# Kernel tuning notes

Measured on AMD Instinct MI355X. Metric: run time of the kernel, lower is better.

Reference implementation:

```python
import jax, jax.numpy as jnp
import numpy as np

IN_FEATURES = 4096
OUT_FEATURES = 4096
LORA_R = 64
LORA_ALPHA = 16
SCALING = LORA_ALPHA / LORA_R  # 0.25


def setup_inputs() -> dict:
    key = jax.random.key(0)
    k_x, k_w, k_s, k_a, k_b = jax.random.split(key, 5)
    x = jax.random.normal(k_x, (4, 2048, IN_FEATURES), dtype=jnp.float32)
    # int8 quantized base weight in [-8, 7] as in the torch buffer init
    weight_quantized = jax.random.randint(k_w, (OUT_FEATURES, IN_FEATURES), -8, 7, dtype=jnp.int8)
    weight_scale = jax.random.normal(k_s, (1,), dtype=jnp.float32)
    lora_A = jax.random.normal(k_a, (LORA_R, IN_FEATURES), dtype=jnp.float32) * 0.01
    # torch init is zeros; use small random values so the LoRA path is exercised
    lora_B = jax.random.normal(k_b, (OUT_FEATURES, LORA_R), dtype=jnp.float32) * 0.01
    return {"x": x, "weight_quantized": weight_quantized, "weight_scale": weight_scale,
            "lora_A": lora_A, "lora_B": lora_B}


def reference(x, weight_quantized, weight_scale, lora_A, lora_B):
    # 1. dequantize base weight on the fly: [out, in]
    w_dequant = weight_quantized.astype(x.dtype) * weight_scale
    # 2. base GEMM: [B, S, in] x [in, out] -> [B, S, out]
    base = jnp.einsum('bsi,oi->bso', x, w_dequant)
    # 3. LoRA low-rank update (dropout is identity in eval mode)
    lora = jnp.einsum('bsr,or->bso', jnp.einsum('bsi,ri->bsr', x, lora_A), lora_B)
    return base + lora * SCALING
```

## Files before the change

kernel.cpp:

```cpp
#include <hip/hip_runtime.h>

#define M_TOT 8192
#define K_TOT 4096
#define N_TOT 4096
#define RANK  64
#define SCALING 0.25f

typedef __bf16 bf16x8 __attribute__((ext_vector_type(8)));
typedef float floatx4 __attribute__((ext_vector_type(4)));
typedef float floatx16 __attribute__((ext_vector_type(16)));
typedef unsigned short ushort8v __attribute__((ext_vector_type(8)));

static __device__ __forceinline__ unsigned short f32_to_bf16(float f) {
  unsigned int u = __float_as_uint(f);
  u += 0x7FFFu + ((u >> 16) & 1u);
  return (unsigned short)(u >> 16);
}

static __device__ __forceinline__ void async_ld16(const void* g, void* l) {
  __builtin_amdgcn_global_load_lds(
      (const __attribute__((address_space(1))) unsigned int*)g,
      (__attribute__((address_space(3))) unsigned int*)l, 16, 0, 0);
}

__global__ __launch_bounds__(256) void cvt_x_kernel(const float4* __restrict__ x,
                                                    ushort8v* __restrict__ xb) {
  int i = blockIdx.x * 256 + threadIdx.x;
  float4 v0 = x[2 * i];
  float4 v1 = x[2 * i + 1];
  ushort8v o;
  o[0] = f32_to_bf16(v0.x); o[1] = f32_to_bf16(v0.y);
  o[2] = f32_to_bf16(v0.z); o[3] = f32_to_bf16(v0.w);
  o[4] = f32_to_bf16(v1.x); o[5] = f32_to_bf16(v1.y);
  o[6] = f32_to_bf16(v1.z); o[7] = f32_to_bf16(v1.w);
  xb[i] = o;
}

__global__ __launch_bounds__(256) void build_weff_kernel(
    const int* __restrict__ wq, const float* __restrict__ scale_p,
    const float* __restrict__ A, const float* __restrict__ B,
    unsigned short* __restrict__ Weff) {
  __shared__ __align__(16) float Bts[64][128];
  __shared__ __align__(16) float As_[64][128];

  const int tid = threadIdx.x;
  const int bo = blockIdx.y * 128;
  const int bk = blockIdx.x * 128;
  const float scale = scale_p[0];

  {
    const int o = tid >> 1;
    const int rh = (tid & 1) * 32;
    const float* gb = B + (size_t)(bo + o) * RANK + rh;
#pragma unroll
    for (int j = 0; j < 8; ++j) {
      float4 v = *(const float4*)(gb + j * 4);
      Bts[rh + j * 4 + 0][o] = v.x;
      Bts[rh + j * 4 + 1][o] = v.y;
      Bts[rh + j * 4 + 2][o] = v.z;
      Bts[rh + j * 4 + 3][o] = v.w;
    }
  }
#pragma unroll
  for (int j = 0; j < 8; ++j) {
    const int ii = j * 1024 + tid * 4;
    const int r = ii >> 7, c = ii & 127;
    *(floatx4*)&As_[r][c] = *(const floatx4*)(A + (size_t)r * K_TOT + bk + c);
  }
  __syncthreads();

  const int to = tid >> 4;
  const int tk = tid & 15;
  float acc[8][8] = {};
#pragma unroll 4
  for (int r = 0; r < RANK; ++r) {
    floatx4 b0 = *(const floatx4*)&Bts[r][to * 8];
    floatx4 b1 = *(const floatx4*)&Bts[r][to * 8 + 4];
    floatx4 a0 = *(const floatx4*)&As_[r][tk * 8];
    floatx4 a1 = *(const floatx4*)&As_[r][tk * 8 + 4];
    float bv[8] = {b0.x, b0.y, b0.z, b0.w, b1.x, b1.y, b1.z, b1.w};
    float av[8] = {a0.x, a0.y, a0.z, a0.w, a1.x, a1.y, a1.z, a1.w};
#pragma unroll
    for (int a = 0; a < 8; ++a)
#pragma unroll
      for (int b = 0; b < 8; ++b) acc[a][b] += bv[a] * av[b];
  }

#pragma unroll
  for (int a = 0; a < 8; ++a) {
    const int o = bo + to * 8 + a;
    const size_t base = (size_t)o * K_TOT + bk + tk * 8;
    const int4 w0 = *(const int4*)(wq + base);
    const int4 w1 = *(const int4*)(wq + base + 4);
    ushort8v st;
    st[0] = f32_to_bf16((float)w0.x * scale + SCALING * acc[a][0]);
    st[1] = f32_to_bf16((float)w0.y * scale + SCALING * acc[a][1]);
    st[2] = f32_to_bf16((float)w0.z * scale + SCALING * acc[a][2]);
    st[3] = f32_to_bf16((float)w0.w * scale + SCALING * acc[a][3]);
    st[4] = f32_to_bf16((float)w1.x * scale + SCALING * acc[a][4]);
    st[5] = f32_to_bf16((float)w1.y * scale + SCALING * acc[a][5]);
    st[6] = f32_to_bf16((float)w1.z * scale + SCALING * acc[a][6]);
    st[7] = f32_to_bf16((float)w1.w * scale + SCALING * acc[a][7]);
    *(ushort8v*)(Weff + base) = st;
  }
}

__global__ __launch_bounds__(512, 2) void gemm_kernel(
    const unsigned short* __restrict__ Xb,
    const unsigned short* __restrict__ Wb,
    float* __restrict__ out) {
  __shared__ __align__(16) unsigned char smem[131072];

  const int tid = threadIdx.x;
  const int lane = tid & 63;
  const int wave = tid >> 6;
  const int wm = wave >> 2;
  const int wn = wave & 3;

  const int bid = blockIdx.x;
  const int swz = (bid & 7) * 64 + (bid >> 3);
  const int bM = (swz >> 4) * 256;
  const int bN = (swz & 15) * 256;

  const int srow = tid >> 3;
  const int scol = ((tid & 7) ^ (srow & 7)) * 8;
  const unsigned short* xs = Xb + (size_t)(bM + srow) * K_TOT + scol;
  const unsigned short* ws = Wb + (size_t)(bN + srow) * K_TOT + scol;

  const int hi = lane >> 5;
  const int l7 = lane & 7;
  const int rb = (lane & 31) * 128;
  const int cc0 = ((0 * 2 + hi) ^ l7) * 16;
  const int cc1 = ((1 * 2 + hi) ^ l7) * 16;
  const int cc2 = ((2 * 2 + hi) ^ l7) * 16;
  const int cc3 = ((3 * 2 + hi) ^ l7) * 16;
  const int aBase = wm * 16384;
  const int bBase = 32768 + wn * 8192;

  floatx16 acc[4][2] = {};
  bf16x8 af[2][2];
  bf16x8 bf[2][4];

#define BAR() asm volatile("s_barrier" ::: "memory")
#define WAIT_LGKM0() asm volatile("s_waitcnt lgkmcnt(0)" ::: "memory")
#define WAIT_VM(N) asm volatile("s_waitcnt vmcnt(" #N ")" ::: "memory")
#define STAGE_A(BUF, H, S, KO)                                              \
  async_ld16(xs + (size_t)((H) * 128 + (S) * 64) * K_TOT + (KO),            \
             smem + (BUF) * 65536 + (H) * 16384 + (S) * 8192 + tid * 16)
#define STAGE_B(BUF, H, S, KO)                                              \
  async_ld16(ws + (size_t)((H) * 128 + (S) * 64) * K_TOT + (KO),            \
             smem + (BUF) * 65536 + 32768 + (H) * 16384 + (S) * 8192 + tid * 16)
#define RD_A(BUF, MI, MM, KK, CC)                                           \
  af[MM][KK] = *(const bf16x8*)(smem + (BUF) * 65536 + aBase + (MI) * 4096 + rb + (CC))
#define RD_B(BUF, NJ, KS, CC)                                               \
  bf[NJ][KS] = *(const bf16x8*)(smem + (BUF) * 65536 + bBase + (NJ) * 4096 + rb + (CC))

#define MFMA_OCT(MB, PB)                                                    \
  {                                                                         \
    _Pragma("unroll") for (int kk = 0; kk < 2; ++kk)                        \
    _Pragma("unroll") for (int mm = 0; mm < 2; ++mm)                        \
    _Pragma("unroll") for (int nn = 0; nn < 2; ++nn)                        \
      acc[(MB) + mm][nn] = __builtin_amdgcn_mfma_f32_32x32x16_bf16(         \
          af[mm][kk], bf[nn][kk + (PB)], acc[(MB) + mm][nn], 0, 0, 0);      \
  }

#define GROUP(BUF, KA, KB)                                                  \
  {                                                                         \
                            \
    RD_B(BUF, 0, 0, cc0); RD_B(BUF, 1, 0, cc0);                             \
    RD_A(BUF, 0, 0, 0, cc0); RD_A(BUF, 1, 1, 0, cc0);                       \
    RD_B(BUF, 0, 1, cc1); RD_B(BUF, 1, 1, cc1);                             \
    RD_A(BUF, 0, 0, 1, cc1); RD_A(BUF, 1, 1, 1, cc1);                       \
    STAGE_A((BUF) ^ 1, 0, 0, KA); STAGE_A((BUF) ^ 1, 0, 1, KA);             \
    __builtin_amdgcn_s_setprio(1);                                          \
    MFMA_OCT(0, 0);                                                         \
    __builtin_amdgcn_s_setprio(0);                                          \
    WAIT_LGKM0(); BAR();                                                    \
                            \
    RD_B(BUF, 0, 2, cc2); RD_B(BUF, 1, 2, cc2);                             \
    RD_A(BUF, 0, 0, 0, cc2); RD_A(BUF, 1, 1, 0, cc2);                       \
    RD_B(BUF, 0, 3, cc3); RD_B(BUF, 1, 3, cc3);                             \
    RD_A(BUF, 0, 0, 1, cc3); RD_A(BUF, 1, 1, 1, cc3);                       \
    STAGE_A((BUF) ^ 1, 1, 0, KA); STAGE_A((BUF) ^ 1, 1, 1, KA);             \
    __builtin_amdgcn_s_setprio(1);                                          \
    MFMA_OCT(0, 2);                                                         \
    __builtin_amdgcn_s_setprio(0);                                          \
    WAIT_LGKM0(); BAR();                                                    \
     \
    RD_A(BUF, 2, 0, 0, cc0); RD_A(BUF, 3, 1, 0, cc0);                       \
    RD_A(BUF, 2, 0, 1, cc1); RD_A(BUF, 3, 1, 1, cc1);                       \
    STAGE_B(BUF, 0, 0, KB); STAGE_B(BUF, 0, 1, KB);                         \
    __builtin_amdgcn_s_setprio(1);                                          \
    MFMA_OCT(2, 0);                                                         \
    __builtin_amdgcn_s_setprio(0);                                          \
    WAIT_LGKM0(); BAR();                                                    \
                 \
    RD_A(BUF, 2, 0, 0, cc2); RD_A(BUF, 3, 1, 0, cc2);                       \
    RD_A(BUF, 2, 0, 1, cc3); RD_A(BUF, 3, 1, 1, cc3);                       \
    STAGE_B(BUF, 1, 0, KB); STAGE_B(BUF, 1, 1, KB);                         \
    __builtin_amdgcn_s_setprio(1);                                          \
    MFMA_OCT(2, 2);                                                         \
    __builtin_amdgcn_s_setprio(0);                                          \
    WAIT_VM(4);                                                             \
    BAR();                                                                  \
  }

  STAGE_A(0, 0, 0, 0); STAGE_A(0, 0, 1, 0);
  STAGE_A(0, 1, 0, 0); STAGE_A(0, 1, 1, 0);
  STAGE_B(0, 0, 0, 0); STAGE_B(0, 0, 1, 0);
  STAGE_B(0, 1, 0, 0); STAGE_B(0, 1, 1, 0);
  STAGE_B(1, 0, 0, 64); STAGE_B(1, 0, 1, 64);
  STAGE_B(1, 1, 0, 64); STAGE_B(1, 1, 1, 64);
  WAIT_VM(0);
  BAR();

  for (int kt = 0; kt < 64; kt += 2) {
    const int ka0 = ((kt + 1) & 63) * 64;
    const int kb0 = ((kt + 2) & 63) * 64;
    const int ka1 = ((kt + 2) & 63) * 64;
    const int kb1 = ((kt + 3) & 63) * 64;
    GROUP(0, ka0, kb0);
    GROUP(1, ka1, kb1);
  }
  WAIT_VM(0);

  const int col0 = bN + wn * 64 + (lane & 31);
#pragma unroll
  for (int mi = 0; mi < 4; ++mi) {
    const int rbase = bM + wm * 128 + mi * 32 + hi * 4;
#pragma unroll
    for (int nj = 0; nj < 2; ++nj) {
#pragma unroll
      for (int rg = 0; rg < 4; ++rg)
#pragma unroll
        for (int rr = 0; rr < 4; ++rr)
          out[(size_t)(rbase + rg * 8 + rr) * N_TOT + (col0 + nj * 32)] =
              acc[mi][nj][rg * 4 + rr];
    }
  }
#undef BAR
#undef WAIT_LGKM0
#undef WAIT_VM
#undef STAGE_A
#undef STAGE_B
#undef RD_A
#undef RD_B
#undef MFMA_OCT
#undef GROUP
}

extern "C" void kernel_launch(void* const* d_in, const int* in_sizes, int n_in,
                              void* d_out, int out_size, void* d_ws, size_t ws_size,
                              hipStream_t stream) {
  const float* x      = (const float*)d_in[0];
  const int*   wq     = (const int*)d_in[1];
  const float* wscale = (const float*)d_in[2];
  const float* lora_A = (const float*)d_in[3];
  const float* lora_B = (const float*)d_in[4];
  float* out = (float*)d_out;

  unsigned short* xb   = (unsigned short*)d_ws;
  unsigned short* weff = (unsigned short*)((char*)d_ws + (size_t)M_TOT * K_TOT * 2);

  cvt_x_kernel<<<16384, 256, 0, stream>>>((const float4*)x, (ushort8v*)xb);
  build_weff_kernel<<<dim3(K_TOT / 128, N_TOT / 128), 256, 0, stream>>>(
      wq, wscale, lora_A, lora_B, weff);
  gemm_kernel<<<512, 512, 0, stream>>>(xb, weff, out);
}
```

Before: 525.9 us.

## Switch GEMM inner loop to 16x16x32 MFMA with two-phase schedule

Replaces the 32x32x16 bf16 MFMA tiling with 16x16x32 MFMAs, giving each wave an 8x4 grid of 16x16 accumulators, and changes the LDS fragment addressing and swizzle offsets to match. The four barrier-separated sub-phases per k-tile become two phases (ALPHA, BETA), each issuing all of its A or B global-to-LDS stages at the start, followed by a larger batch of LDS reads and MFMAs. The aim is fewer barriers and better MFMA issue density per synchronisation. In exchange it performs more LDS reads per MFMA and needs more fragment registers, which could hurt occupancy or increase LDS bandwidth pressure.

```diff
diff --git a/kernel.cpp b/kernel.cpp
--- a/kernel.cpp
+++ b/kernel.cpp
@@ -8,7 +8,6 @@
 
 typedef __bf16 bf16x8 __attribute__((ext_vector_type(8)));
 typedef float floatx4 __attribute__((ext_vector_type(4)));
-typedef float floatx16 __attribute__((ext_vector_type(16)));
 typedef unsigned short ushort8v __attribute__((ext_vector_type(8)));
 
 static __device__ __forceinline__ unsigned short f32_to_bf16(float f) {
@@ -105,6 +104,21 @@
   }
 }
 
+
+template <int QM>
+static __device__ __forceinline__ void mfma_half(floatx4 (&acc)[8][4],
+                                                 const bf16x8 (&af)[4][2],
+                                                 const bf16x8 (&bf)[4][2]) {
+#pragma unroll
+  for (int ks = 0; ks < 2; ++ks)
+#pragma unroll
+    for (int i = 0; i < 4; ++i)
+#pragma unroll
+      for (int j = 0; j < 4; ++j)
+        acc[QM * 4 + i][j] = __builtin_amdgcn_mfma_f32_16x16x32_bf16(
+            af[i][ks], bf[j][ks], acc[QM * 4 + i][j], 0, 0, 0);
+}
+
 __global__ __launch_bounds__(512, 2) void gemm_kernel(
     const unsigned short* __restrict__ Xb,
     const unsigned short* __restrict__ Wb,
@@ -127,19 +141,15 @@
   const unsigned short* xs = Xb + (size_t)(bM + srow) * K_TOT + scol;
   const unsigned short* ws = Wb + (size_t)(bN + srow) * K_TOT + scol;
 
-  const int hi = lane >> 5;
-  const int l7 = lane & 7;
-  const int rb = (lane & 31) * 128;
-  const int cc0 = ((0 * 2 + hi) ^ l7) * 16;
-  const int cc1 = ((1 * 2 + hi) ^ l7) * 16;
-  const int cc2 = ((2 * 2 + hi) ^ l7) * 16;
-  const int cc3 = ((3 * 2 + hi) ^ l7) * 16;
+  const int rb = (lane & 15) * 128;
+  const int c0 = (((lane >> 4) + 0) ^ (lane & 7)) * 16;
+  const int c1 = (((lane >> 4) + 4) ^ (lane & 7)) * 16;
   const int aBase = wm * 16384;
   const int bBase = 32768 + wn * 8192;
 
-  floatx16 acc[4][2] = {};
-  bf16x8 af[2][2];
-  bf16x8 bf[2][4];
+  floatx4 acc[8][4] = {};
+  bf16x8 af[4][2];
+  bf16x8 bf[4][2];
 
 #define BAR() asm volatile("s_barrier" ::: "memory")
 #define WAIT_LGKM0() asm volatile("s_waitcnt lgkmcnt(0)" ::: "memory")
@@ -150,59 +160,43 @@
 #define STAGE_B(BUF, H, S, KO)                                              \
   async_ld16(ws + (size_t)((H) * 128 + (S) * 64) * K_TOT + (KO),            \
              smem + (BUF) * 65536 + 32768 + (H) * 16384 + (S) * 8192 + tid * 16)
-#define RD_A(BUF, MI, MM, KK, CC)                                           \
-  af[MM][KK] = *(const bf16x8*)(smem + (BUF) * 65536 + aBase + (MI) * 4096 + rb + (CC))
-#define RD_B(BUF, NJ, KS, CC)                                               \
-  bf[NJ][KS] = *(const bf16x8*)(smem + (BUF) * 65536 + bBase + (NJ) * 4096 + rb + (CC))
-
-#define MFMA_OCT(MB, PB)                                                    \
+#define DSR_A(BUF, QM, II, KS)                                              \
+  af[II][KS] = *(const bf16x8*)(smem + (BUF) * 65536 + aBase +              \
+                                ((QM) * 4 + (II)) * 2048 + rb + ((KS) ? c1 : c0))
+#define DSR_B(BUF, J, KS)                                                   \
+  bf[J][KS] = *(const bf16x8*)(smem + (BUF) * 65536 + bBase +               \
+                               (J) * 2048 + rb + ((KS) ? c1 : c0))
+
+#define ALPHA(BUF, KA)                                                      \
   {                                                                         \
-    _Pragma("unroll") for (int kk = 0; kk < 2; ++kk)                        \
-    _Pragma("unroll") for (int mm = 0; mm < 2; ++mm)                        \
-    _Pragma("unroll") for (int nn = 0; nn < 2; ++nn)                        \
-      acc[(MB) + mm][nn] = __builtin_amdgcn_mfma_f32_32x32x16_bf16(         \
-          af[mm][kk], bf[nn][kk + (PB)], acc[(MB) + mm][nn], 0, 0, 0);      \
-  }
-
-#define GROUP(BUF, KA, KB)                                                  \
-  {                                                                         \
-                            \
-    RD_B(BUF, 0, 0, cc0); RD_B(BUF, 1, 0, cc0);                             \
-    RD_A(BUF, 0, 0, 0, cc0); RD_A(BUF, 1, 1, 0, cc0);                       \
-    RD_B(BUF, 0, 1, cc1); RD_B(BUF, 1, 1, cc1);                             \
-    RD_A(BUF, 0, 0, 1, cc1); RD_A(BUF, 1, 1, 1, cc1);                       \
     STAGE_A((BUF) ^ 1, 0, 0, KA); STAGE_A((BUF) ^ 1, 0, 1, KA);             \
+    STAGE_A((BUF) ^ 1, 1, 0, KA); STAGE_A((BUF) ^ 1, 1, 1, KA);             \
+    DSR_B(BUF, 0, 0); DSR_B(BUF, 1, 0);                                     \
+    DSR_A(BUF, 0, 0, 0); DSR_A(BUF, 0, 1, 0);                               \
+    DSR_B(BUF, 2, 0); DSR_B(BUF, 3, 0);                                     \
+    DSR_A(BUF, 0, 2, 0); DSR_A(BUF, 0, 3, 0);                               \
+    DSR_B(BUF, 0, 1); DSR_B(BUF, 1, 1);                                     \
+    DSR_A(BUF, 0, 0, 1); DSR_A(BUF, 0, 1, 1);                               \
+    DSR_B(BUF, 2, 1); DSR_B(BUF, 3, 1);                                     \
+    DSR_A(BUF, 0, 2, 1); DSR_A(BUF, 0, 3, 1);                               \
     __builtin_amdgcn_s_setprio(1);                                          \
-    MFMA_OCT(0, 0);                                                         \
+    mfma_half<0>(acc, af, bf);                                              \
     __builtin_amdgcn_s_setprio(0);                                          \
     WAIT_LGKM0(); BAR();                                                    \
-                            \
-    RD_B(BUF, 0, 2, cc2); RD_B(BUF, 1, 2, cc2);                             \
-    RD_A(BUF, 0, 0, 0, cc2); RD_A(BUF, 1, 1, 0, cc2);                       \
-    RD_B(BUF, 0, 3, cc3); RD_B(BUF, 1, 3, cc3);                             \
-    RD_A(BUF, 0, 0, 1, cc3); RD_A(BUF, 1, 1, 1, cc3);                       \
-    STAGE_A((BUF) ^ 1, 1, 0, KA); STAGE_A((BUF) ^ 1, 1, 1, KA);             \
+  }
+
+#define BETA(BUF, KB)                                                       \
+  {                                                                         \
+    STAGE_B(BUF, 0, 0, KB); STAGE_B(BUF, 0, 1, KB);                         \
+    STAGE_B(BUF, 1, 0, KB); STAGE_B(BUF, 1, 1, KB);                         \
+    DSR_A(BUF, 1, 0, 0); DSR_A(BUF, 1, 1, 0);                               \
+    DSR_A(BUF, 1, 2, 0); DSR_A(BUF, 1, 3, 0);                               \
+    DSR_A(BUF, 1, 0, 1); DSR_A(BUF, 1, 1, 1);                               \
+    DSR_A(BUF, 1, 2, 1); DSR_A(BUF, 1, 3, 1);                               \
     __builtin_amdgcn_s_setprio(1);                                          \
-    MFMA_OCT(0, 2);                                                         \
+    mfma_half<1>(acc, af, bf);                                              \
     __builtin_amdgcn_s_setprio(0);                                          \
-    WAIT_LGKM0(); BAR();                                                    \
-     \
-    RD_A(BUF, 2, 0, 0, cc0); RD_A(BUF, 3, 1, 0, cc0);                       \
-    RD_A(BUF, 2, 0, 1, cc1); RD_A(BUF, 3, 1, 1, cc1);                       \
-    STAGE_B(BUF, 0, 0, KB); STAGE_B(BUF, 0, 1, KB);                         \
-    __builtin_amdgcn_s_setprio(1);                                          \
-    MFMA_OCT(2, 0);                                                         \
-    __builtin_amdgcn_s_setprio(0);                                          \
-    WAIT_LGKM0(); BAR();                                                    \
-                 \
-    RD_A(BUF, 2, 0, 0, cc2); RD_A(BUF, 3, 1, 0, cc2);                       \
-    RD_A(BUF, 2, 0, 1, cc3); RD_A(BUF, 3, 1, 1, cc3);                       \
-    STAGE_B(BUF, 1, 0, KB); STAGE_B(BUF, 1, 1, KB);                         \
-    __builtin_amdgcn_s_setprio(1);                                          \
-    MFMA_OCT(2, 2);                                                         \
-    __builtin_amdgcn_s_setprio(0);                                          \
-    WAIT_VM(4);                                                             \
-    BAR();                                                                  \
+    WAIT_LGKM0(); WAIT_VM(4); BAR();                                        \
   }
 
   STAGE_A(0, 0, 0, 0); STAGE_A(0, 0, 1, 0);
@@ -219,23 +213,21 @@
     const int kb0 = ((kt + 2) & 63) * 64;
     const int ka1 = ((kt + 2) & 63) * 64;
     const int kb1 = ((kt + 3) & 63) * 64;
-    GROUP(0, ka0, kb0);
-    GROUP(1, ka1, kb1);
+    ALPHA(0, ka0); BETA(0, kb0);
+    ALPHA(1, ka1); BETA(1, kb1);
   }
   WAIT_VM(0);
 
-  const int col0 = bN + wn * 64 + (lane & 31);
-#pragma unroll
-  for (int mi = 0; mi < 4; ++mi) {
-    const int rbase = bM + wm * 128 + mi * 32 + hi * 4;
-#pragma unroll
-    for (int nj = 0; nj < 2; ++nj) {
-#pragma unroll
-      for (int rg = 0; rg < 4; ++rg)
-#pragma unroll
-        for (int rr = 0; rr < 4; ++rr)
-          out[(size_t)(rbase + rg * 8 + rr) * N_TOT + (col0 + nj * 32)] =
-              acc[mi][nj][rg * 4 + rr];
+  const int row0 = bM + wm * 128 + ((lane >> 4) << 2);
+  const int col0 = bN + wn * 64 + (lane & 15);
+#pragma unroll
+  for (int i = 0; i < 8; ++i) {
+#pragma unroll
+    for (int j = 0; j < 4; ++j) {
+#pragma unroll
+      for (int r = 0; r < 4; ++r) {
+        out[(size_t)(row0 + i * 16 + r) * N_TOT + (col0 + j * 16)] = acc[i][j][r];
+      }
     }
   }
 #undef BAR
@@ -243,10 +235,10 @@
 #undef WAIT_VM
 #undef STAGE_A
 #undef STAGE_B
-#undef RD_A
-#undef RD_B
-#undef MFMA_OCT
-#undef GROUP
+#undef DSR_A
+#undef DSR_B
+#undef ALPHA
+#undef BETA
 }
 
 extern "C" void kernel_launch(void* const* d_in, const int* in_sizes, int n_in,
```

Result: faster. 496.1 us (-5.7%).
